# Kernel tuning notes

Measured on AMD Instinct MI355X. Metric: run time of the kernel, lower is better.

## Reference

```python
import jax, jax.numpy as jnp
import numpy as np

BSZ, SEQ, EMBED = 2, 4096, 1024
NUM_HEADS = 16
HEAD_DIM = EMBED // NUM_HEADS
WINDOW = 256  # attention_window[layer_id]


def setup_inputs() -> dict:
    key = jax.random.key(0)
    ks = jax.random.split(key, 7)
    s = 1.0 / np.sqrt(EMBED)
    return {
        "hidden_states": jax.random.normal(ks[0], (BSZ, SEQ, EMBED), jnp.float32),
        "Wq": jax.random.normal(ks[1], (EMBED, EMBED), jnp.float32) * s,
        "bq": jnp.zeros((EMBED,), jnp.float32),
        "Wk": jax.random.normal(ks[2], (EMBED, EMBED), jnp.float32) * s,
        "bk": jnp.zeros((EMBED,), jnp.float32),
        "Wv": jax.random.normal(ks[3], (EMBED, EMBED), jnp.float32) * s,
        "bv": jnp.zeros((EMBED,), jnp.float32),
    }


def _blocks3(x, nb, w):
    # x: [b, s + 2w, h, d] -> [b, nb, 3w, h, d]; block c sees key blocks c-1, c, c+1
    b = x.shape[0]
    xb = x.reshape(b, nb + 2, w, NUM_HEADS, HEAD_DIM)
    return jnp.concatenate([xb[:, i:i + nb] for i in range(3)], axis=2)


def reference(hidden_states, Wq, bq, Wk, bk, Wv, bv):
    b, s, e = hidden_states.shape
    w = WINDOW
    nb = s // w
    q = (hidden_states @ Wq + bq) * (1.0 / np.sqrt(HEAD_DIM))
    k = hidden_states @ Wk + bk
    v = hidden_states @ Wv + bv
    q = q.reshape(b, nb, w, NUM_HEADS, HEAD_DIM)
    k = k.reshape(b, s, NUM_HEADS, HEAD_DIM)
    v = v.reshape(b, s, NUM_HEADS, HEAD_DIM)
    pad = ((0, 0), (w, w), (0, 0), (0, 0))
    kb = _blocks3(jnp.pad(k, pad), nb, w)  # [b, nb, 3w, h, d]
    vb = _blocks3(jnp.pad(v, pad), nb, w)
    # banded scores: query x in block n attends keys at global pos n*w - w + y
    scores = jnp.einsum('bnxhd,bnyhd->bnhxy', q, kb)  # [b, nb, h, w, 3w]
    x_idx = jnp.arange(w)
    y_idx = jnp.arange(3 * w)
    band = jnp.abs(y_idx[None, :] - x_idx[:, None] - w) <= w  # [w, 3w]
    kpos = jnp.arange(nb)[:, None] * w - w + y_idx[None, :]   # [nb, 3w]
    inb = (kpos >= 0) & (kpos < s)
    mask = band[None, :, :] & inb[:, None, :]                 # [nb, w, 3w]
    scores = jnp.where(mask[None, :, None, :, :], scores, -jnp.inf)
    probs = jax.nn.softmax(scores.astype(jnp.float32), axis=-1).astype(v.dtype)
    attn = jnp.einsum('bnhxy,bnyhd->bnxhd', probs, vb)        # [b, nb, w, h, d]
    return attn.reshape(b, s, e)
```

## Files before the change

### kernel.cpp

```cpp
#include <hip/hip_runtime.h>
#include <stdint.h>

#define SEQ    4096
#define EMBED  1024
#define NHEAD  16
#define HDIM   64
#define WIN    256
#define BSZ    2
#define M_TOT  (BSZ * SEQ)
#define N_QKV  3072
#define N_QK   2048
#define K_DIM  1024
#define LOG2E  1.4426950408889634f

typedef __attribute__((ext_vector_type(8))) __bf16 bf16x8;
typedef __attribute__((ext_vector_type(4))) float  f32x4;

__device__ __forceinline__ unsigned short f2bf(float f) {
  union { float f; unsigned int u; } c; c.f = f;
  unsigned int u = c.u;
  unsigned int r = (u + 0x7FFFu + ((u >> 16) & 1u)) >> 16;
  return (unsigned short)r;
}

__device__ __forceinline__ unsigned int cvt_pk_bf16(float lo, float hi) {
  unsigned int r;
  asm("v_cvt_pk_bf16_f32 %0, %1, %2" : "=v"(r) : "v"(lo), "v"(hi));
  return r;
}

__device__ __forceinline__ void gl2lds16(const void* g, void* l) {
  __builtin_amdgcn_global_load_lds((const __attribute__((address_space(1))) void*)g,
                                   (__attribute__((address_space(3))) void*)l, 16, 0, 0);
}

__global__ __launch_bounds__(256) void cvt_all(const float* __restrict__ in,
                                               unsigned short* __restrict__ out,
                                               const float* __restrict__ Wq,
                                               const float* __restrict__ Wk,
                                               const float* __restrict__ Wv,
                                               unsigned short* __restrict__ Wt) {
  __shared__ float t[32][33];
  int tid = threadIdx.x;
  if (blockIdx.x < 8192) {
    int i = (blockIdx.x * 256 + tid) * 4;
    float4 v = *(const float4*)(in + i);
    ushort4 o;
    o.x = f2bf(v.x); o.y = f2bf(v.y); o.z = f2bf(v.z); o.w = f2bf(v.w);
    *(ushort4*)(out + i) = o;
  } else {
    int wb = blockIdx.x - 8192;
    int z  = wb >> 10;
    int rem = wb & 1023;
    int kb = (rem & 31) * 32, nb = (rem >> 5) * 32;
    const float* W = (z == 0) ? Wq : (z == 1) ? Wk : Wv;
    int tx = tid & 31, ty = tid >> 5;
    for (int it = 0; it < 4; ++it) {
      int k = kb + ty + it * 8;
      t[ty + it * 8][tx] = W[(size_t)k * 1024 + nb + tx];
    }
    __syncthreads();
    for (int it = 0; it < 4; ++it) {
      int n = nb + ty + it * 8;
      Wt[(size_t)(z * 1024 + n) * 1024 + kb + tx] = f2bf(t[tx][ty + it * 8]);
    }
  }
}

__global__ __launch_bounds__(512, 2) void qkv_gemm(const unsigned short* __restrict__ A,
                                                   const unsigned short* __restrict__ Bt,
                                                   const float* __restrict__ bq,
                                                   const float* __restrict__ bk,
                                                   const float* __restrict__ bv,
                                                   unsigned short* __restrict__ C,
                                                   unsigned short* __restrict__ Vt) {
  __shared__ unsigned short As[2][128 * 64];
  __shared__ unsigned short Bs[2][256 * 64];
  int tid  = threadIdx.x;
  int lane = tid & 63, wave = tid >> 6;
  int ln   = lane & 15, quad = lane >> 4;
  int flat = blockIdx.y * 12 + blockIdx.x;
  int swz  = (flat & 7) * 96 + (flat >> 3);
  int m0 = (swz / 12) * 128, n0 = (swz % 12) * 256;
  int wy = wave >> 2, wx = wave & 3;
  f32x4 acc[4][4];
#pragma unroll
  for (int i = 0; i < 4; ++i)
#pragma unroll
    for (int j = 0; j < 4; ++j) acc[i][j] = (f32x4){0.f, 0.f, 0.f, 0.f};

  int c8 = tid & 7;
  int sRow[2];
#pragma unroll
  for (int s = 0; s < 2; ++s) sRow[s] = s * 64 + (tid >> 3);

#define STG_A(buf, kt)                                                           \
  do {                                                                           \
    _Pragma("unroll")                                                            \
    for (int s = 0; s < 2; ++s) {                                                \
      int lr = sRow[s]; int cg = c8 ^ (lr & 7);                                  \
      gl2lds16(A + (size_t)(m0 + lr) * K_DIM + (kt) * 64 + cg * 8,               \
               &As[buf][lr * 512 + c8 * 8]);                                     \
    }                                                                            \
  } while (0)
#define STG_BLO(buf, kt)                                                         \
  do {                                                                           \
    _Pragma("unroll")                                                            \
    for (int s = 0; s < 2; ++s) {                                                \
      int lr = sRow[s]; int cg = c8 ^ (lr & 7);                                  \
      gl2lds16(Bt + (size_t)(n0 + lr) * K_DIM + (kt) * 64 + cg * 8,              \
               &Bs[buf][lr * 512 + c8 * 8]);                                     \
    }                                                                            \
  } while (0)
#define STG_BHI(buf, kt)                                                         \
  do {                                                                           \
    _Pragma("unroll")                                                            \
    for (int s = 0; s < 2; ++s) {                                                \
      int lr = sRow[s]; int cg = c8 ^ (lr & 7);                                  \
      gl2lds16(Bt + (size_t)(n0 + 128 + lr) * K_DIM + (kt) * 64 + cg * 8,        \
               &Bs[buf][128 * 512 + lr * 512 + c8 * 8]);                         \
    }                                                                            \
  } while (0)

#undef STG_A
#undef STG_BLO
#undef STG_BHI
#define STG_A(buf, kt)                                                           \
  do {                                                                           \
    _Pragma("unroll")                                                            \
    for (int s = 0; s < 2; ++s) {                                                \
      int lr = sRow[s]; int cg = c8 ^ (lr & 7);                                  \
      gl2lds16(A + (size_t)(m0 + lr) * K_DIM + (kt) * 64 + cg * 8,               \
               &As[buf][lr * 64 + c8 * 8]);                                      \
    }                                                                            \
  } while (0)
#define STG_BLO(buf, kt)                                                         \
  do {                                                                           \
    _Pragma("unroll")                                                            \
    for (int s = 0; s < 2; ++s) {                                                \
      int lr = sRow[s]; int cg = c8 ^ (lr & 7);                                  \
      gl2lds16(Bt + (size_t)(n0 + lr) * K_DIM + (kt) * 64 + cg * 8,              \
               &Bs[buf][lr * 64 + c8 * 8]);                                      \
    }                                                                            \
  } while (0)
#define STG_BHI(buf, kt)                                                         \
  do {                                                                           \
    _Pragma("unroll")                                                            \
    for (int s = 0; s < 2; ++s) {                                                \
      int lr = sRow[s]; int cg = c8 ^ (lr & 7);                                  \
      gl2lds16(Bt + (size_t)(n0 + 128 + lr) * K_DIM + (kt) * 64 + cg * 8,        \
               &Bs[buf][(128 + lr) * 64 + c8 * 8]);                              \
    }                                                                            \
  } while (0)

  STG_A(0, 0); STG_BLO(0, 0); STG_BHI(0, 0);
  STG_A(1, 1); STG_BLO(1, 1);
  asm volatile("s_waitcnt vmcnt(4)" ::: "memory");
  __builtin_amdgcn_s_barrier();

  bf16x8 af[4][2], bv0[2][2], bv1[2][2];
  int aBase = wy * 64, bBase = wx * 64;

#pragma unroll 1
  for (int t = 0; t < 16; ++t) {
    int cur = t & 1;
    const unsigned short* as = As[cur];
    const unsigned short* bs = Bs[cur];

#pragma unroll
    for (int i2 = 0; i2 < 4; ++i2) {
      int row = aBase + i2 * 16 + ln;
#pragma unroll
      for (int ks = 0; ks < 2; ++ks) {
        int c = (ks * 4 + quad) ^ (row & 7);
        af[i2][ks] = *(const bf16x8*)&as[row * 64 + c * 8];
      }
    }
#pragma unroll
    for (int j2 = 0; j2 < 2; ++j2) {
      int row = bBase + j2 * 16 + ln;
#pragma unroll
      for (int ks = 0; ks < 2; ++ks) {
        int c = (ks * 4 + quad) ^ (row & 7);
        bv0[j2][ks] = *(const bf16x8*)&bs[row * 64 + c * 8];
      }
    }
    if (t < 15) STG_BHI(cur ^ 1, t + 1);
    __builtin_amdgcn_s_barrier();
    __builtin_amdgcn_s_setprio(1);
#pragma unroll
    for (int ks = 0; ks < 2; ++ks)
#pragma unroll
      for (int i2 = 0; i2 < 4; ++i2)
#pragma unroll
        for (int j2 = 0; j2 < 2; ++j2)
          acc[i2][j2] = __builtin_amdgcn_mfma_f32_16x16x32_bf16(af[i2][ks], bv0[j2][ks], acc[i2][j2], 0, 0, 0);
    __builtin_amdgcn_s_setprio(0);
    __builtin_amdgcn_s_barrier();

#pragma unroll
    for (int j2 = 0; j2 < 2; ++j2) {
      int row = bBase + 32 + j2 * 16 + ln;
#pragma unroll
      for (int ks = 0; ks < 2; ++ks) {
        int c = (ks * 4 + quad) ^ (row & 7);
        bv1[j2][ks] = *(const bf16x8*)&bs[row * 64 + c * 8];
      }
    }
    if (t < 14) { STG_A(cur, t + 2); STG_BLO(cur, t + 2); }
    __builtin_amdgcn_s_barrier();
    __builtin_amdgcn_s_setprio(1);
#pragma unroll
    for (int ks = 0; ks < 2; ++ks)
#pragma unroll
      for (int i2 = 0; i2 < 4; ++i2)
#pragma unroll
        for (int j2 = 0; j2 < 2; ++j2)
          acc[i2][2 + j2] = __builtin_amdgcn_mfma_f32_16x16x32_bf16(af[i2][ks], bv1[j2][ks], acc[i2][2 + j2], 0, 0, 0);
    __builtin_amdgcn_s_setprio(0);
    if (t < 14) asm volatile("s_waitcnt vmcnt(4)" ::: "memory");
    else        asm volatile("s_waitcnt vmcnt(0)" ::: "memory");
    __builtin_amdgcn_s_barrier();
  }
#undef STG_A
#undef STG_BLO
#undef STG_BHI

  if (n0 < N_QK) {
#pragma unroll
    for (int j = 0; j < 4; ++j) {
      int n = n0 + wx * 64 + j * 16 + ln;
      float bias, scl;
      if (n < 1024) { bias = bq[n];        scl = 0.125f * LOG2E; }
      else          { bias = bk[n - 1024]; scl = 1.f; }
#pragma unroll
      for (int i = 0; i < 4; ++i) {
        int mb = m0 + wy * 64 + i * 16 + quad * 4;
#pragma unroll
        for (int r = 0; r < 4; ++r) {
          float v = (acc[i][j][r] + bias) * scl;
          C[(size_t)(mb + r) * N_QK + n] = f2bf(v);
        }
      }
    }
  } else {
#pragma unroll
    for (int j = 0; j < 4; ++j) {
      int n  = n0 + wx * 64 + j * 16 + ln;
      int hd = n - 2048;
      float bias = bv[hd];
#pragma unroll
      for (int i = 0; i < 4; ++i) {
        int mb  = m0 + wy * 64 + i * 16 + quad * 4;
        int bb  = mb >> 12;
        int pos = mb & (SEQ - 1);
        ushort4 pk;
        pk.x = f2bf(acc[i][j][0] + bias);
        pk.y = f2bf(acc[i][j][1] + bias);
        pk.z = f2bf(acc[i][j][2] + bias);
        pk.w = f2bf(acc[i][j][3] + bias);
        *(ushort4*)&Vt[((size_t)bb * (NHEAD * HDIM) + hd) * SEQ + pos] = pk;
      }
    }
  }
}

__global__ __launch_bounds__(256) void attn(const unsigned short* __restrict__ qk,
                                            const unsigned short* __restrict__ vtg,
                                            float* __restrict__ out) {
  __shared__ unsigned short Kl[64 * 72];
  __shared__ unsigned short Vl[64 * 72];
  int tid  = threadIdx.x;
  int lane = tid & 63, wave = tid >> 6;
  int ln   = lane & 15, quad = lane >> 4;
  int bx = blockIdx.x;
  int lx = ((bx & 7) << 3) | (bx >> 3);
  int q0 = lx * 64, head = blockIdx.y, b = blockIdx.z;
  size_t baseRow = (size_t)b * SEQ;
  const unsigned short* kptr = qk + 1024;
  const unsigned short* vrow = vtg + ((size_t)(b * NHEAD + head) * HDIM) * SEQ;

  int sy = tid >> 3, sc = tid & 7;
  const unsigned short* kbase = kptr + (baseRow + sy) * (size_t)N_QK + head * HDIM + sc * 8;
  const unsigned short* vbase = vrow + (size_t)sy * SEQ + sc * 8;

  bf16x8 qf[2];
  {
    size_t ro = (baseRow + q0 + wave * 16 + ln) * (size_t)N_QK + head * HDIM + quad * 8;
    qf[0] = *(const bf16x8*)&qk[ro];
    qf[1] = *(const bf16x8*)&qk[ro + 32];
  }

  float l_st = 0.f;
  f32x4 o_acc[4];
  for (int dt = 0; dt < 4; ++dt) o_acc[dt] = (f32x4){0.f, 0.f, 0.f, 0.f};

  int lo = (q0 >= 256) ? 0 : (256 - q0) / 64;
  int hi = (SEQ + 256 - q0) / 64; if (hi > 9) hi = 9;

  uint4 pk0, pk1, pv0, pv1;
#define PREFETCH(KT)                                                        \
  {                                                                         \
    pk0 = *(const uint4*)&kbase[(size_t)(KT) * N_QK];                       \
    pk1 = *(const uint4*)&kbase[(size_t)((KT) + 32) * N_QK];                \
    pv0 = *(const uint4*)&vbase[(KT)];                                      \
    pv1 = *(const uint4*)&vbase[(size_t)32 * SEQ + (KT)];                   \
  }

  PREFETCH(q0 - 256 + lo * 64);

  int srcA = ((lane & 16) << 1) | ln;
  int srcB = srcA + 16;
  bool hiQ = (lane & 32) != 0;

  for (int t = lo; t < hi; ++t) {
    int kt = q0 - 256 + t * 64;
    __syncthreads();
    *(uint4*)&Kl[sy * 72 + sc * 8]        = pk0;
    *(uint4*)&Kl[(sy + 32) * 72 + sc * 8] = pk1;
    *(uint4*)&Vl[sy * 72 + sc * 8]        = pv0;
    *(uint4*)&Vl[(sy + 32) * 72 + sc * 8] = pv1;
    __syncthreads();

    if (t + 1 < hi) { PREFETCH(kt + 64); }

    f32x4 s[4];
    __builtin_amdgcn_s_setprio(1);
    for (int nt = 0; nt < 4; ++nt) {
      bf16x8 kf0 = *(const bf16x8*)&Kl[(nt * 16 + ln) * 72 + quad * 8];
      bf16x8 kf1 = *(const bf16x8*)&Kl[(nt * 16 + ln) * 72 + 32 + quad * 8];
      f32x4 z = (f32x4){0.f, 0.f, 0.f, 0.f};
      z = __builtin_amdgcn_mfma_f32_16x16x32_bf16(kf0, qf[0], z, 0, 0, 0);
      z = __builtin_amdgcn_mfma_f32_16x16x32_bf16(kf1, qf[1], z, 0, 0, 0);
      s[nt] = z;
    }
    __builtin_amdgcn_s_setprio(0);

    if (t == 0 || t == 8) {
      int qq = q0 + wave * 16 + ln;
      for (int nt = 0; nt < 4; ++nt) {
        int kb = kt + nt * 16 + quad * 4 - qq;
        for (int r = 0; r < 4; ++r) {
          int dd = kb + r;
          if (dd < -WIN || dd > WIN) s[nt][r] = -INFINITY;
        }
      }
    }

    float rs = 0.f;
    for (int nt = 0; nt < 4; ++nt)
      for (int r = 0; r < 4; ++r) {
        float p = exp2f(s[nt][r]);
        s[nt][r] = p;
        rs += p;
      }
    l_st += rs;

    unsigned int p01[4], p23[4];
    for (int nt = 0; nt < 4; ++nt) {
      p01[nt] = cvt_pk_bf16(s[nt][0], s[nt][1]);
      p23[nt] = cvt_pk_bf16(s[nt][2], s[nt][3]);
    }

    for (int ks = 0; ks < 2; ++ks) {
      int ntA = 2 * ks, ntB = 2 * ks + 1;
      unsigned int a0 = (unsigned int)__shfl((int)p01[ntA], srcA);
      unsigned int a1 = (unsigned int)__shfl((int)p23[ntA], srcA);
      unsigned int a2 = (unsigned int)__shfl((int)p01[ntA], srcB);
      unsigned int a3 = (unsigned int)__shfl((int)p23[ntA], srcB);
      unsigned int b0 = (unsigned int)__shfl((int)p01[ntB], srcA);
      unsigned int b1 = (unsigned int)__shfl((int)p23[ntB], srcA);
      unsigned int b2 = (unsigned int)__shfl((int)p01[ntB], srcB);
      unsigned int b3 = (unsigned int)__shfl((int)p23[ntB], srcB);
      union { uint4 u; bf16x8 v; } pf;
      pf.u.x = hiQ ? b0 : a0;
      pf.u.y = hiQ ? b1 : a1;
      pf.u.z = hiQ ? b2 : a2;
      pf.u.w = hiQ ? b3 : a3;
      __builtin_amdgcn_s_setprio(1);
      for (int dt = 0; dt < 4; ++dt) {
        bf16x8 vf = *(const bf16x8*)&Vl[(dt * 16 + ln) * 72 + ks * 32 + quad * 8];
        o_acc[dt] = __builtin_amdgcn_mfma_f32_16x16x32_bf16(vf, pf.v, o_acc[dt], 0, 0, 0);
      }
      __builtin_amdgcn_s_setprio(0);
    }
  }

  float l = l_st;
  l += __shfl_xor(l, 16);
  l += __shfl_xor(l, 32);
  float inv = 1.0f / l;
  int qpos = q0 + wave * 16 + ln;
  float* ob = out + (baseRow + qpos) * (size_t)EMBED + head * HDIM + quad * 4;
  for (int dt = 0; dt < 4; ++dt) {
    float4 v;
    v.x = o_acc[dt][0] * inv;
    v.y = o_acc[dt][1] * inv;
    v.z = o_acc[dt][2] * inv;
    v.w = o_acc[dt][3] * inv;
    *(float4*)(ob + dt * 16) = v;
  }
#undef PREFETCH
}

extern "C" void kernel_launch(void* const* d_in, const int* in_sizes, int n_in,
                              void* d_out, int out_size, void* d_ws, size_t ws_size,
                              hipStream_t stream) {
  const float* h  = (const float*)d_in[0];
  const float* Wq = (const float*)d_in[1];
  const float* bq = (const float*)d_in[2];
  const float* Wk = (const float*)d_in[3];
  const float* bk = (const float*)d_in[4];
  const float* Wv = (const float*)d_in[5];
  const float* bv = (const float*)d_in[6];
  float* out = (float*)d_out;

  unsigned short* h_bf  = (unsigned short*)d_ws;
  unsigned short* wt_bf = h_bf + (size_t)M_TOT * K_DIM;
  unsigned short* qk    = wt_bf + (size_t)N_QKV * K_DIM;
  unsigned short* vtg   = qk + (size_t)M_TOT * N_QK;

  cvt_all<<<8192 + 3072, 256, 0, stream>>>(h, h_bf, Wq, Wk, Wv, wt_bf);
  qkv_gemm<<<dim3(12, 64), 512, 0, stream>>>(h_bf, wt_bf, bq, bk, bv, qk, vtg);
  attn<<<dim3(SEQ / 64, NHEAD, BSZ), 256, 0, stream>>>(qk, vtg, out);
}
```

Before: 207.3 us.

## Triple-buffer QKV GEMM LDS stages and drop intra-iteration barriers

Switches the QKV GEMM from a double-buffered LDS pipeline with split A/B-low/B-high staging and three barriers per k-step to a triple-buffered ring. Each k-step's full A+B tile is prefetched two iterations ahead and only one barrier is kept per iteration. Buffer pointers rotate at the end of each step. The aim is to cut barrier stalls and improve overlap of global-to-LDS copies with MFMA work. In exchange, LDS use per block grows by half, which could limit occupancy.

```diff
diff --git a/kernel.cpp b/kernel.cpp
--- a/kernel.cpp
+++ b/kernel.cpp
@@ -74,8 +74,8 @@
                                                    const float* __restrict__ bv,
                                                    unsigned short* __restrict__ C,
                                                    unsigned short* __restrict__ Vt) {
-  __shared__ unsigned short As[2][128 * 64];
-  __shared__ unsigned short Bs[2][256 * 64];
+  __shared__ unsigned short As[3][128 * 64];
+  __shared__ unsigned short Bs[3][256 * 64];
   int tid  = threadIdx.x;
   int lane = tid & 63, wave = tid >> 6;
   int ln   = lane & 15, quad = lane >> 4;
@@ -89,91 +89,44 @@
 #pragma unroll
     for (int j = 0; j < 4; ++j) acc[i][j] = (f32x4){0.f, 0.f, 0.f, 0.f};
 
-  int c8 = tid & 7;
-  int sRow[2];
-#pragma unroll
-  for (int s = 0; s < 2; ++s) sRow[s] = s * 64 + (tid >> 3);
-
-#define STG_A(buf, kt)                                                           \
+#define STAGE(asW, bsW, kt)                                                      \
   do {                                                                           \
     _Pragma("unroll")                                                            \
     for (int s = 0; s < 2; ++s) {                                                \
-      int lr = sRow[s]; int cg = c8 ^ (lr & 7);                                  \
-      gl2lds16(A + (size_t)(m0 + lr) * K_DIM + (kt) * 64 + cg * 8,               \
-               &As[buf][lr * 512 + c8 * 8]);                                     \
+      int ch = s * 512 + tid; int r = ch >> 3, c = ch & 7, cg = c ^ (r & 7);     \
+      gl2lds16(A + (size_t)(m0 + r) * K_DIM + (size_t)(kt) * 64 + cg * 8,        \
+               (asW) + ch * 8);                                                  \
+    }                                                                            \
+    _Pragma("unroll")                                                            \
+    for (int s = 0; s < 4; ++s) {                                                \
+      int ch = s * 512 + tid; int r = ch >> 3, c = ch & 7, cg = c ^ (r & 7);     \
+      gl2lds16(Bt + (size_t)(n0 + r) * K_DIM + (size_t)(kt) * 64 + cg * 8,       \
+               (bsW) + ch * 8);                                                  \
     }                                                                            \
   } while (0)
-#define STG_BLO(buf, kt)                                                         \
-  do {                                                                           \
-    _Pragma("unroll")                                                            \
-    for (int s = 0; s < 2; ++s) {                                                \
-      int lr = sRow[s]; int cg = c8 ^ (lr & 7);                                  \
-      gl2lds16(Bt + (size_t)(n0 + lr) * K_DIM + (kt) * 64 + cg * 8,              \
-               &Bs[buf][lr * 512 + c8 * 8]);                                     \
-    }                                                                            \
-  } while (0)
-#define STG_BHI(buf, kt)                                                         \
-  do {                                                                           \
-    _Pragma("unroll")                                                            \
-    for (int s = 0; s < 2; ++s) {                                                \
-      int lr = sRow[s]; int cg = c8 ^ (lr & 7);                                  \
-      gl2lds16(Bt + (size_t)(n0 + 128 + lr) * K_DIM + (kt) * 64 + cg * 8,        \
-               &Bs[buf][128 * 512 + lr * 512 + c8 * 8]);                         \
-    }                                                                            \
-  } while (0)
-
-#undef STG_A
-#undef STG_BLO
-#undef STG_BHI
-#define STG_A(buf, kt)                                                           \
-  do {                                                                           \
-    _Pragma("unroll")                                                            \
-    for (int s = 0; s < 2; ++s) {                                                \
-      int lr = sRow[s]; int cg = c8 ^ (lr & 7);                                  \
-      gl2lds16(A + (size_t)(m0 + lr) * K_DIM + (kt) * 64 + cg * 8,               \
-               &As[buf][lr * 64 + c8 * 8]);                                      \
-    }                                                                            \
-  } while (0)
-#define STG_BLO(buf, kt)                                                         \
-  do {                                                                           \
-    _Pragma("unroll")                                                            \
-    for (int s = 0; s < 2; ++s) {                                                \
-      int lr = sRow[s]; int cg = c8 ^ (lr & 7);                                  \
-      gl2lds16(Bt + (size_t)(n0 + lr) * K_DIM + (kt) * 64 + cg * 8,              \
-               &Bs[buf][lr * 64 + c8 * 8]);                                      \
-    }                                                                            \
-  } while (0)
-#define STG_BHI(buf, kt)                                                         \
-  do {                                                                           \
-    _Pragma("unroll")                                                            \
-    for (int s = 0; s < 2; ++s) {                                                \
-      int lr = sRow[s]; int cg = c8 ^ (lr & 7);                                  \
-      gl2lds16(Bt + (size_t)(n0 + 128 + lr) * K_DIM + (kt) * 64 + cg * 8,        \
-               &Bs[buf][(128 + lr) * 64 + c8 * 8]);                              \
-    }                                                                            \
-  } while (0)
-
-  STG_A(0, 0); STG_BLO(0, 0); STG_BHI(0, 0);
-  STG_A(1, 1); STG_BLO(1, 1);
-  asm volatile("s_waitcnt vmcnt(4)" ::: "memory");
+
+  unsigned short *pa0 = As[0], *pa1 = As[1], *pa2 = As[2];
+  unsigned short *pb0 = Bs[0], *pb1 = Bs[1], *pb2 = Bs[2];
+
+  STAGE(pa0, pb0, 0);
+  STAGE(pa1, pb1, 1);
+  asm volatile("s_waitcnt vmcnt(6)" ::: "memory");
   __builtin_amdgcn_s_barrier();
 
-  bf16x8 af[4][2], bv0[2][2], bv1[2][2];
   int aBase = wy * 64, bBase = wx * 64;
 
 #pragma unroll 1
   for (int t = 0; t < 16; ++t) {
-    int cur = t & 1;
-    const unsigned short* as = As[cur];
-    const unsigned short* bs = Bs[cur];
-
+    if (t < 14) STAGE(pa2, pb2, t + 2);
+
+    bf16x8 af[4][2], bf0[2][2], bf1[2][2];
 #pragma unroll
     for (int i2 = 0; i2 < 4; ++i2) {
       int row = aBase + i2 * 16 + ln;
 #pragma unroll
       for (int ks = 0; ks < 2; ++ks) {
         int c = (ks * 4 + quad) ^ (row & 7);
-        af[i2][ks] = *(const bf16x8*)&as[row * 64 + c * 8];
+        af[i2][ks] = *(const bf16x8*)&pa0[row * 64 + c * 8];
       }
     }
 #pragma unroll
@@ -182,11 +135,9 @@
 #pragma unroll
       for (int ks = 0; ks < 2; ++ks) {
         int c = (ks * 4 + quad) ^ (row & 7);
-        bv0[j2][ks] = *(const bf16x8*)&bs[row * 64 + c * 8];
-      }
-    }
-    if (t < 15) STG_BHI(cur ^ 1, t + 1);
-    __builtin_amdgcn_s_barrier();
+        bf0[j2][ks] = *(const bf16x8*)&pb0[row * 64 + c * 8];
+      }
+    }
     __builtin_amdgcn_s_setprio(1);
 #pragma unroll
     for (int ks = 0; ks < 2; ++ks)
@@ -194,21 +145,17 @@
       for (int i2 = 0; i2 < 4; ++i2)
 #pragma unroll
         for (int j2 = 0; j2 < 2; ++j2)
-          acc[i2][j2] = __builtin_amdgcn_mfma_f32_16x16x32_bf16(af[i2][ks], bv0[j2][ks], acc[i2][j2], 0, 0, 0);
+          acc[i2][j2] = __builtin_amdgcn_mfma_f32_16x16x32_bf16(af[i2][ks], bf0[j2][ks], acc[i2][j2], 0, 0, 0);
     __builtin_amdgcn_s_setprio(0);
-    __builtin_amdgcn_s_barrier();
-
 #pragma unroll
     for (int j2 = 0; j2 < 2; ++j2) {
       int row = bBase + 32 + j2 * 16 + ln;
 #pragma unroll
       for (int ks = 0; ks < 2; ++ks) {
         int c = (ks * 4 + quad) ^ (row & 7);
-        bv1[j2][ks] = *(const bf16x8*)&bs[row * 64 + c * 8];
-      }
-    }
-    if (t < 14) { STG_A(cur, t + 2); STG_BLO(cur, t + 2); }
-    __builtin_amdgcn_s_barrier();
+        bf1[j2][ks] = *(const bf16x8*)&pb0[row * 64 + c * 8];
+      }
+    }
     __builtin_amdgcn_s_setprio(1);
 #pragma unroll
     for (int ks = 0; ks < 2; ++ks)
@@ -216,15 +163,18 @@
       for (int i2 = 0; i2 < 4; ++i2)
 #pragma unroll
         for (int j2 = 0; j2 < 2; ++j2)
-          acc[i2][2 + j2] = __builtin_amdgcn_mfma_f32_16x16x32_bf16(af[i2][ks], bv1[j2][ks], acc[i2][2 + j2], 0, 0, 0);
+          acc[i2][2 + j2] = __builtin_amdgcn_mfma_f32_16x16x32_bf16(af[i2][ks], bf1[j2][ks], acc[i2][2 + j2], 0, 0, 0);
     __builtin_amdgcn_s_setprio(0);
-    if (t < 14) asm volatile("s_waitcnt vmcnt(4)" ::: "memory");
+
+    if (t < 14) asm volatile("s_waitcnt vmcnt(6)" ::: "memory");
     else        asm volatile("s_waitcnt vmcnt(0)" ::: "memory");
     __builtin_amdgcn_s_barrier();
-  }
-#undef STG_A
-#undef STG_BLO
-#undef STG_BHI
+
+    unsigned short* tp;
+    tp = pa0; pa0 = pa1; pa1 = pa2; pa2 = tp;
+    tp = pb0; pb0 = pb1; pb1 = pb2; pb2 = tp;
+  }
+#undef STAGE
 
   if (n0 < N_QK) {
 #pragma unroll
```

After: 217.3 us. 1.05x slower.
